# Kernel tuning notes

Hardware: AMD Instinct MI355X
Metric: run time of the kernel (lower is better)

## Reference

```python
import math
import jax, jax.numpy as jnp
import numpy as np

G, PQ, PV = 12, 4, 8

def setup_inputs() -> dict:
    key = jax.random.key(0)
    ks = jax.random.split(key, 14)
    N, L, Cn, Ce, Ch = 1, 512, 384, 128, 192
    Node = jax.random.normal(ks[0], (N, L, Cn), jnp.float32)
    Edge = jax.random.normal(ks[1], (N, L, L, Ce), jnp.float32)
    # proper rotation matrices via QR of random gaussians
    raw = jax.random.normal(ks[2], (N, L, 3, 3), jnp.float32)
    rots, _ = jnp.linalg.qr(raw)
    trans = jax.random.normal(ks[3], (N, L, 3), jnp.float32) * 10.0
    def lin(k, fan_in, fan_out):
        return jax.random.normal(k, (fan_in, fan_out), jnp.float32) / np.sqrt(fan_in)
    return {
        'Node': Node, 'Edge': Edge, 'rots': rots, 'trans': trans,
        'Wq': lin(ks[4], Cn, Ch), 'Wk': lin(ks[5], Cn, Ch), 'Wv': lin(ks[6], Cn, Ch),
        'Wqv': lin(ks[7], Cn, 3 * G * PQ), 'Wkv': lin(ks[8], Cn, 3 * G * PQ),
        'Wvv': lin(ks[9], Cn, 3 * G * PV), 'Wbias': lin(ks[10], Ce, G),
        'gamma': jnp.zeros((G,), jnp.float32),
        'Wout': lin(ks[11], Ce * G + Ch + G * PV * 4, Cn),
        'bout': jnp.zeros((Cn,), jnp.float32),
    }

def reference(Node, Edge, rots, trans, Wq, Wk, Wv, Wqv, Wkv, Wvv, Wbias, gamma, Wout, bout):
    N, L, Cn = Node.shape
    Ce = Edge.shape[-1]
    Ch = Wq.shape[1]
    ppg = Ch // G
    t = trans / 10.0  # Frame(T.rots, T.trans / 10.0)
    q = (Node @ Wq).reshape(N, L, G, ppg)
    k = (Node @ Wk).reshape(N, L, G, ppg)
    v = (Node @ Wv).reshape(N, L, G, ppg)
    qv = (Node @ Wqv).reshape(N, L, G, PQ, 3)
    kv = (Node @ Wkv).reshape(N, L, G, PQ, 3)
    vv = (Node @ Wvv).reshape(N, L, G, PV, 3)
    apply_frame = lambda p: jnp.einsum('nlij,nlgpj->nlgpi', rots, p) + t[:, :, None, None]
    qv = apply_frame(qv)
    kv = apply_frame(kv)
    vv = apply_frame(vv)
    # pairwise squared point distances, summed over xyz and query points -> [N,L,L,G]
    d = qv[:, :, None] - kv[:, None]
    sq = jnp.sum(d * d, axis=(-1, -2))
    bias = jnp.einsum('nijc,cg->nijg', Edge, Wbias)
    WC = math.sqrt(2.0 / 9.0 / PQ)
    WL = math.sqrt(1.0 / 3.0)
    attn = jnp.einsum('nlgc,nmgc->nlmg', q, k) / math.sqrt(ppg) + bias
    attn = attn - jax.nn.softplus(gamma) * (WC / 2.0) * sq
    attn = jax.nn.softmax(WL * attn, axis=2)  # softmax over key index m
    O_Edge = jnp.einsum('nijg,nijc->nigc', attn, Edge).reshape(N, L, G * Ce)
    O_Node = jnp.einsum('nijg,njgc->nigc', attn, v).reshape(N, L, Ch)
    O_vec = jnp.einsum('nijg,njgpc->nigpc', attn, vv)
    # invert_apply: R^T (x - t)
    O_vec = jnp.einsum('nlji,nlgpj->nlgpi', rots, O_vec - t[:, :, None, None])
    O_norm = jnp.sqrt(jnp.sum(O_vec * O_vec, axis=-1) + 1e-8).reshape(N, L, -1)
    O_vec = O_vec.reshape(N, L, -1)
    feat = jnp.concatenate([O_Edge, O_Node, O_vec, O_norm], axis=-1)
    return feat @ Wout + bout
```

## Files before the change

### kernel.cpp

```cpp
#include <hip/hip_runtime.h>
#include <math.h>

#define LQ 512
#define CN 384
#define CE 128
#define CH 192
#define NG 12
#define PPG 16
#define FEAT 2112
#define NPROJ 1152
#define WLs 0.5773502691896258f

#define WS_RAW  0u
#define WS_QVG  589824u
#define WS_KVT  663552u
#define WS_VVG  737280u
#define WS_QN   884736u
#define WS_KNT  890880u
#define WS_KT   897024u
#define WS_ATT  995328u
#define WS_FEAT 4141056u
#define WS_PART 5222400u
#define WS_PM   5812224u
#define WS_PS   5824512u

__global__ __launch_bounds__(256) void k1a_gemm(
    const float* __restrict__ Node,
    const float* __restrict__ Wq, const float* __restrict__ Wk,
    const float* __restrict__ Wv, const float* __restrict__ Wqv,
    const float* __restrict__ Wkv, const float* __restrict__ Wvv,
    float* __restrict__ ws)
{
    __shared__ float As[64][68];
    __shared__ float Bs[64][48];
    const int tid = threadIdx.x;
    const int cb = blockIdx.x % 24;
    const int l0 = (blockIdx.x / 24) * 64;
    const int col0 = cb * 48;

    const float* W; int nc, lc0;
    if (col0 < 192)      { W = Wq;  nc = 192; lc0 = col0; }
    else if (col0 < 384) { W = Wk;  nc = 192; lc0 = col0 - 192; }
    else if (col0 < 576) { W = Wv;  nc = 192; lc0 = col0 - 384; }
    else if (col0 < 720) { W = Wqv; nc = 144; lc0 = col0 - 576; }
    else if (col0 < 864) { W = Wkv; nc = 144; lc0 = col0 - 720; }
    else                 { W = Wvv; nc = 288; lc0 = col0 - 864; }

    const int tx = tid & 15, ty = tid >> 4;
    float acc[4][3];
#pragma unroll
    for (int r = 0; r < 4; ++r)
#pragma unroll
        for (int c = 0; c < 3; ++c) acc[r][c] = 0.f;

    for (int kc = 0; kc < 6; ++kc) {
        __syncthreads();
#pragma unroll
        for (int pass = 0; pass < 4; ++pass) {
            int m = (tid >> 4) + pass * 16;
            int kk = (tid & 15) * 4;
            const float4 a = *(const float4*)(Node + (size_t)(l0 + m) * CN + kc * 64 + kk);
            As[kk + 0][m] = a.x; As[kk + 1][m] = a.y;
            As[kk + 2][m] = a.z; As[kk + 3][m] = a.w;
        }
#pragma unroll
        for (int p = 0; p < 12; ++p) {
            int idx = p * 256 + tid;
            int kk = idx / 48, c = idx - kk * 48;
            Bs[kk][c] = W[(size_t)(kc * 64 + kk) * nc + lc0 + c];
        }
        __syncthreads();
#pragma unroll 8
        for (int kk = 0; kk < 64; ++kk) {
            const float4 av = *(const float4*)&As[kk][tx * 4];
            const float b0 = Bs[kk][ty * 3 + 0];
            const float b1 = Bs[kk][ty * 3 + 1];
            const float b2 = Bs[kk][ty * 3 + 2];
            acc[0][0] = fmaf(av.x, b0, acc[0][0]); acc[0][1] = fmaf(av.x, b1, acc[0][1]); acc[0][2] = fmaf(av.x, b2, acc[0][2]);
            acc[1][0] = fmaf(av.y, b0, acc[1][0]); acc[1][1] = fmaf(av.y, b1, acc[1][1]); acc[1][2] = fmaf(av.y, b2, acc[1][2]);
            acc[2][0] = fmaf(av.z, b0, acc[2][0]); acc[2][1] = fmaf(av.z, b1, acc[2][1]); acc[2][2] = fmaf(av.z, b2, acc[2][2]);
            acc[3][0] = fmaf(av.w, b0, acc[3][0]); acc[3][1] = fmaf(av.w, b1, acc[3][1]); acc[3][2] = fmaf(av.w, b2, acc[3][2]);
        }
    }
    float* raw = ws + WS_RAW;
#pragma unroll
    for (int r = 0; r < 4; ++r)
#pragma unroll
        for (int c = 0; c < 3; ++c)
            raw[(size_t)(l0 + tx * 4 + r) * NPROJ + col0 + ty * 3 + c] = acc[r][c];
    if (col0 >= 192 && col0 < 384) {
#pragma unroll
        for (int r = 0; r < 4; ++r)
#pragma unroll
            for (int c = 0; c < 3; ++c)
                ws[WS_KT + (size_t)(col0 - 192 + ty * 3 + c) * LQ + l0 + tx * 4 + r] = acc[r][c];
    }
}

__global__ __launch_bounds__(256) void k1b_vec(
    const float* __restrict__ rots, const float* __restrict__ trans,
    float* __restrict__ ws)
{
    __shared__ float sqbuf[96];
    const int tid = threadIdx.x;
    const int l = blockIdx.x;
    const float* raw = ws + WS_RAW + (size_t)l * NPROJ;

    if (tid < 192) {
        int src, pt, typ;
        if (tid < 48)      { typ = 0; pt = tid;      src = 576 + pt * 3; }
        else if (tid < 96) { typ = 1; pt = tid - 48; src = 720 + pt * 3; }
        else               { typ = 2; pt = tid - 96; src = 864 + pt * 3; }
        float v0 = raw[src], v1 = raw[src + 1], v2 = raw[src + 2];
        const float* R = rots + l * 9;
        float o0 = R[0] * v0 + R[1] * v1 + R[2] * v2 + trans[l * 3 + 0] * 0.1f;
        float o1 = R[3] * v0 + R[4] * v1 + R[5] * v2 + trans[l * 3 + 1] * 0.1f;
        float o2 = R[6] * v0 + R[7] * v1 + R[8] * v2 + trans[l * 3 + 2] * 0.1f;
        if (typ == 0) {
            float* dst = ws + WS_QVG + (size_t)l * 144 + pt * 3;
            dst[0] = o0; dst[1] = o1; dst[2] = o2;
        } else if (typ == 1) {
            ws[WS_KVT + (size_t)(pt * 3 + 0) * LQ + l] = o0;
            ws[WS_KVT + (size_t)(pt * 3 + 1) * LQ + l] = o1;
            ws[WS_KVT + (size_t)(pt * 3 + 2) * LQ + l] = o2;
        } else {
            float* dst = ws + WS_VVG + (size_t)l * 288 + pt * 3;
            dst[0] = o0; dst[1] = o1; dst[2] = o2;
        }
        if (tid < 96) sqbuf[tid] = o0 * o0 + o1 * o1 + o2 * o2;
    }
    __syncthreads();
    if (tid < 24) {
        int typ = tid / 12, g = tid % 12;
        int b = typ * 48 + g * 4;
        float s = sqbuf[b] + sqbuf[b + 1] + sqbuf[b + 2] + sqbuf[b + 3];
        if (typ == 0) ws[WS_QN + (size_t)l * 12 + g] = s;
        else          ws[WS_KNT + (size_t)g * LQ + l] = s;
    }
}

__global__ __launch_bounds__(256, 4) void k2_attn(
    const float* __restrict__ Edge, const float* __restrict__ Wbias,
    const float* __restrict__ gamma, float* __restrict__ ws)
{
    __shared__ float et[256 * 33];
    __shared__ float cgls[NG];
    __shared__ float red[4][NG];
    const int tid = threadIdx.x;
    const int i = blockIdx.x >> 1;
    const int h = blockIdx.x & 1;
    const int j = h * 256 + tid;

    if (tid < NG)
        cgls[tid] = log1pf(__expf(gamma[tid])) * 0.11785113019775793f;

    const float4* e4 = (const float4*)Edge + ((size_t)i * LQ + h * 256) * 32;
    float4 buf[8];
#pragma unroll
    for (int kk = 0; kk < 8; ++kk) {
        int idx = kk * 256 + tid;
        buf[kk] = e4[(size_t)(idx >> 3) * 32 + (idx & 7)];
    }
    __syncthreads();

    float lgs[NG];
    {
        const float* qrow  = ws + WS_RAW + (size_t)i * NPROJ;
        const float* qvrow = ws + WS_QVG + (size_t)i * 144;
        const float* qnrow = ws + WS_QN  + (size_t)i * NG;
        const float* KT  = ws + WS_KT;
        const float* KVT = ws + WS_KVT;
        const float* KNT = ws + WS_KNT;
#pragma unroll
        for (int g = 0; g < NG; ++g) {
            float qk = 0.f;
#pragma unroll
            for (int u = 0; u < PPG; ++u)
                qk = fmaf(qrow[g * PPG + u], KT[(size_t)(g * PPG + u) * LQ + j], qk);
            float dt = 0.f;
#pragma unroll
            for (int u = 0; u < 12; ++u)
                dt = fmaf(qvrow[g * 12 + u], KVT[(size_t)(g * 12 + u) * LQ + j], dt);
            float sq = qnrow[g] + KNT[(size_t)g * LQ + j] - 2.f * dt;
            lgs[g] = qk * 0.25f - cgls[g] * sq;
        }
    }

#pragma unroll
    for (int kk = 0; kk < 8; ++kk) {
        int idx = kk * 256 + tid;
        float* d = et + (idx >> 3) * 33 + (idx & 7) * 4;
        d[0] = buf[kk].x; d[1] = buf[kk].y; d[2] = buf[kk].z; d[3] = buf[kk].w;
    }
    __syncthreads();

    for (int ch = 0; ch < 4; ++ch) {
        if (ch < 3) {
#pragma unroll
            for (int kk = 0; kk < 8; ++kk) {
                int idx = kk * 256 + tid;
                buf[kk] = e4[(size_t)(idx >> 3) * 32 + (ch + 1) * 8 + (idx & 7)];
            }
        }
        const float* wbch = Wbias + ch * 32 * NG;
        const float* r0 = et + tid * 33;
#pragma unroll 4
        for (int c = 0; c < 32; ++c) {
            float e0 = r0[c];
            const float* wb = wbch + c * NG;
#pragma unroll
            for (int g = 0; g < NG; ++g) lgs[g] = fmaf(e0, wb[g], lgs[g]);
        }
        __syncthreads();
        if (ch < 3) {
#pragma unroll
            for (int kk = 0; kk < 8; ++kk) {
                int idx = kk * 256 + tid;
                float* d = et + (idx >> 3) * 33 + (idx & 7) * 4;
                d[0] = buf[kk].x; d[1] = buf[kk].y; d[2] = buf[kk].z; d[3] = buf[kk].w;
            }
            __syncthreads();
        }
    }

    const int wid = tid >> 6, lane = tid & 63;
    float pm[NG];
#pragma unroll
    for (int g = 0; g < NG; ++g) pm[g] = lgs[g];
#pragma unroll
    for (int g = 0; g < NG; ++g)
        for (int off = 1; off < 64; off <<= 1)
            pm[g] = fmaxf(pm[g], __shfl_xor(pm[g], off));
    if (lane == 0) {
#pragma unroll
        for (int g = 0; g < NG; ++g) red[wid][g] = pm[g];
    }
    __syncthreads();
    float gm[NG];
#pragma unroll
    for (int g = 0; g < NG; ++g)
        gm[g] = fmaxf(fmaxf(red[0][g], red[1][g]), fmaxf(red[2][g], red[3][g]));
    if (tid < NG)
        ws[WS_PM + ((size_t)i * 2 + h) * NG + tid] =
            fmaxf(fmaxf(red[0][tid], red[1][tid]), fmaxf(red[2][tid], red[3][tid]));
    __syncthreads();

    float ps[NG];
#pragma unroll
    for (int g = 0; g < NG; ++g) {
        float e = __expf(WLs * (lgs[g] - gm[g]));
        lgs[g] = e;
        ps[g] = e;
    }
#pragma unroll
    for (int g = 0; g < NG; ++g)
        for (int off = 1; off < 64; off <<= 1)
            ps[g] += __shfl_xor(ps[g], off);
    if (lane == 0) {
#pragma unroll
        for (int g = 0; g < NG; ++g) red[wid][g] = ps[g];
    }
    __syncthreads();
    if (tid < NG)
        ws[WS_PS + ((size_t)i * 2 + h) * NG + tid] =
            red[0][tid] + red[1][tid] + red[2][tid] + red[3][tid];

    float* attT = ws + WS_ATT + (size_t)i * (NG * LQ);
#pragma unroll
    for (int g = 0; g < NG; ++g) attT[g * LQ + j] = lgs[g];
}

__global__ __launch_bounds__(256) void k3a_oedge(
    const float* __restrict__ Edge, float* __restrict__ ws)
{
    __shared__ float atls[NG * 516];
    __shared__ float bufA[4][32][NG][4];
    __shared__ float sc[2][NG];
    const int tid = threadIdx.x;
    const int qi = blockIdx.x;

    if (tid < 24) {
        int hh = tid / NG, g = tid % NG;
        float m0 = ws[WS_PM + ((size_t)qi * 2 + 0) * NG + g];
        float m1 = ws[WS_PM + ((size_t)qi * 2 + 1) * NG + g];
        float ss0 = ws[WS_PS + ((size_t)qi * 2 + 0) * NG + g];
        float ss1 = ws[WS_PS + ((size_t)qi * 2 + 1) * NG + g];
        float m = fmaxf(m0, m1);
        float e0 = __expf(WLs * (m0 - m));
        float e1 = __expf(WLs * (m1 - m));
        float denom = ss0 * e0 + ss1 * e1;
        sc[hh][g] = (hh ? e1 : e0) / denom;
    }
    __syncthreads();

    const float4* attT4 = (const float4*)(ws + WS_ATT + (size_t)qi * (NG * LQ));
#pragma unroll
    for (int m = 0; m < 6; ++m) {
        int idx = m * 256 + tid;
        int g = idx >> 7, j4 = idx & 127;
        float s = sc[j4 >> 6][g];
        float4 v = attT4[g * 128 + j4];
        v.x *= s; v.y *= s; v.z *= s; v.w *= s;
        *(float4*)&atls[g * 516 + j4 * 4] = v;
    }
    __syncthreads();

    const int w = tid >> 6, lane = tid & 63, jh = lane >> 5, c4 = lane & 31;
    float acc[NG][4];
#pragma unroll
    for (int g = 0; g < NG; ++g)
#pragma unroll
        for (int r = 0; r < 4; ++r) acc[g][r] = 0.f;
    const float4* e4 = (const float4*)(Edge + (size_t)qi * LQ * CE);
    for (int s = 0; s < 16; ++s) {
        int j0 = w * 128 + jh * 64 + s * 4;
        float4 e0 = e4[(size_t)(j0 + 0) * 32 + c4];
        float4 e1 = e4[(size_t)(j0 + 1) * 32 + c4];
        float4 e2 = e4[(size_t)(j0 + 2) * 32 + c4];
        float4 e3 = e4[(size_t)(j0 + 3) * 32 + c4];
#pragma unroll
        for (int g = 0; g < NG; ++g) {
            float4 a = *(const float4*)&atls[g * 516 + j0];
            acc[g][0] = fmaf(a.x, e0.x, fmaf(a.y, e1.x, fmaf(a.z, e2.x, fmaf(a.w, e3.x, acc[g][0]))));
            acc[g][1] = fmaf(a.x, e0.y, fmaf(a.y, e1.y, fmaf(a.z, e2.y, fmaf(a.w, e3.y, acc[g][1]))));
            acc[g][2] = fmaf(a.x, e0.z, fmaf(a.y, e1.z, fmaf(a.z, e2.z, fmaf(a.w, e3.z, acc[g][2]))));
            acc[g][3] = fmaf(a.x, e0.w, fmaf(a.y, e1.w, fmaf(a.z, e2.w, fmaf(a.w, e3.w, acc[g][3]))));
        }
    }
#pragma unroll
    for (int g = 0; g < NG; ++g)
#pragma unroll
        for (int r = 0; r < 4; ++r) acc[g][r] += __shfl_xor(acc[g][r], 32);
    if (jh == 0) {
#pragma unroll
        for (int g = 0; g < NG; ++g)
#pragma unroll
            for (int r = 0; r < 4; ++r) bufA[w][c4][g][r] = acc[g][r];
    }
    __syncthreads();
    float* feat = ws + WS_FEAT + (size_t)qi * FEAT;
    for (int m = 0; m < 6; ++m) {
        int o = tid + m * 256;
        int g = o >> 7, c = o & 127;
        int cc4 = c >> 2, r = c & 3;
        feat[o] = bufA[0][cc4][g][r] + bufA[1][cc4][g][r] +
                  bufA[2][cc4][g][r] + bufA[3][cc4][g][r];
    }
}

__global__ __launch_bounds__(256) void k3b_rest(
    const float* __restrict__ rots, const float* __restrict__ trans,
    float* __restrict__ ws)
{
    __shared__ float atls[NG * 516];
    __shared__ float sc[2][NG];
    __shared__ float ovecl[240];
    const int tid = threadIdx.x;
    const int qi = blockIdx.x >> 1;
    const int s  = blockIdx.x & 1;

    if (tid < 24) {
        int hh = tid / NG, g = tid % NG;
        float m0 = ws[WS_PM + ((size_t)qi * 2 + 0) * NG + g];
        float m1 = ws[WS_PM + ((size_t)qi * 2 + 1) * NG + g];
        float ss0 = ws[WS_PS + ((size_t)qi * 2 + 0) * NG + g];
        float ss1 = ws[WS_PS + ((size_t)qi * 2 + 1) * NG + g];
        float m = fmaxf(m0, m1);
        float e0 = __expf(WLs * (m0 - m));
        float e1 = __expf(WLs * (m1 - m));
        float denom = ss0 * e0 + ss1 * e1;
        sc[hh][g] = (hh ? e1 : e0) / denom;
    }
    __syncthreads();

    const float4* attT4 = (const float4*)(ws + WS_ATT + (size_t)qi * (NG * LQ));
#pragma unroll
    for (int m = 0; m < 6; ++m) {
        int idx = m * 256 + tid;
        int g = idx >> 7, j4 = idx & 127;
        float f = sc[j4 >> 6][g];
        float4 v = attT4[g * 128 + j4];
        v.x *= f; v.y *= f; v.z *= f; v.w *= f;
        *(float4*)&atls[g * 516 + j4 * 4] = v;
    }
    __syncthreads();

    float* feat = ws + WS_FEAT + (size_t)qi * FEAT;
    const float* raw = ws + WS_RAW;
    const float* vvg = ws + WS_VVG;
    if (tid < 240) {
        if (s == 0 && tid < 192) {
            int g = tid >> 4;
            const float* arow = atls + g * 516;
            float sum = 0.f;
            for (int j4 = 0; j4 < 128; ++j4) {
                float4 a = *(const float4*)&arow[j4 * 4];
                int j = j4 * 4;
                sum = fmaf(a.x, raw[(size_t)(j + 0) * NPROJ + 384 + tid], sum);
                sum = fmaf(a.y, raw[(size_t)(j + 1) * NPROJ + 384 + tid], sum);
                sum = fmaf(a.z, raw[(size_t)(j + 2) * NPROJ + 384 + tid], sum);
                sum = fmaf(a.w, raw[(size_t)(j + 3) * NPROJ + 384 + tid], sum);
            }
            feat[1536 + tid] = sum;
        } else {
            int u = (s == 0) ? (tid - 192) : (48 + tid);
            int lidx = (s == 0) ? (tid - 192) : tid;
            int g = u / 24;
            const float* arow = atls + g * 516;
            float sum = 0.f;
            for (int j4 = 0; j4 < 128; ++j4) {
                float4 a = *(const float4*)&arow[j4 * 4];
                int j = j4 * 4;
                sum = fmaf(a.x, vvg[(size_t)(j + 0) * 288 + u], sum);
                sum = fmaf(a.y, vvg[(size_t)(j + 1) * 288 + u], sum);
                sum = fmaf(a.z, vvg[(size_t)(j + 2) * 288 + u], sum);
                sum = fmaf(a.w, vvg[(size_t)(j + 3) * 288 + u], sum);
            }
            ovecl[lidx] = sum;
        }
    }
    __syncthreads();

    int npts = (s == 0) ? 16 : 80;
    if (tid < npts) {
        int P = (s == 0) ? tid : (16 + tid);
        int u0l = (s == 0) ? (P * 3) : (P * 3 - 48);
        const float* R = rots + qi * 9;
        float t0 = trans[qi * 3 + 0] * 0.1f;
        float t1 = trans[qi * 3 + 1] * 0.1f;
        float t2 = trans[qi * 3 + 2] * 0.1f;
        float d0 = ovecl[u0l + 0] - t0;
        float d1 = ovecl[u0l + 1] - t1;
        float d2 = ovecl[u0l + 2] - t2;
        float o0 = R[0] * d0 + R[3] * d1 + R[6] * d2;
        float o1 = R[1] * d0 + R[4] * d1 + R[7] * d2;
        float o2 = R[2] * d0 + R[5] * d1 + R[8] * d2;
        feat[1728 + P * 3 + 0] = o0;
        feat[1728 + P * 3 + 1] = o1;
        feat[1728 + P * 3 + 2] = o2;
        feat[2016 + P] = sqrtf(o0 * o0 + o1 * o1 + o2 * o2 + 1e-8f);
    }
}

__global__ __launch_bounds__(256) void k4_gemm(const float* __restrict__ Wout,
                                               float* __restrict__ ws)
{
    __shared__ float As[64][68];
    __shared__ float Bs[64][48];
    const int tid = threadIdx.x;
    const int cc = blockIdx.x >> 6;
    const int t  = blockIdx.x & 63;
    const int l0 = (t >> 3) * 64;
    const int col0 = (t & 7) * 48;
    const float* feat = ws + WS_FEAT;

    const int tx = tid & 15, ty = tid >> 4;
    float acc[4][3];
#pragma unroll
    for (int r = 0; r < 4; ++r)
#pragma unroll
        for (int c = 0; c < 3; ++c) acc[r][c] = 0.f;

    for (int kc = cc * 11; kc < cc * 11 + 11; ++kc) {
        __syncthreads();
#pragma unroll
        for (int pass = 0; pass < 4; ++pass) {
            int m = (tid >> 4) + pass * 16;
            int kk = (tid & 15) * 4;
            const float4 a = *(const float4*)(feat + (size_t)(l0 + m) * FEAT + kc * 64 + kk);
            As[kk + 0][m] = a.x; As[kk + 1][m] = a.y;
            As[kk + 2][m] = a.z; As[kk + 3][m] = a.w;
        }
#pragma unroll
        for (int p = 0; p < 12; ++p) {
            int idx = p * 256 + tid;
            int kk = idx / 48, c = idx - kk * 48;
            Bs[kk][c] = Wout[(size_t)(kc * 64 + kk) * CN + col0 + c];
        }
        __syncthreads();
#pragma unroll 8
        for (int kk = 0; kk < 64; ++kk) {
            const float4 av = *(const float4*)&As[kk][tx * 4];
            const float b0 = Bs[kk][ty * 3 + 0];
            const float b1 = Bs[kk][ty * 3 + 1];
            const float b2 = Bs[kk][ty * 3 + 2];
            acc[0][0] = fmaf(av.x, b0, acc[0][0]); acc[0][1] = fmaf(av.x, b1, acc[0][1]); acc[0][2] = fmaf(av.x, b2, acc[0][2]);
            acc[1][0] = fmaf(av.y, b0, acc[1][0]); acc[1][1] = fmaf(av.y, b1, acc[1][1]); acc[1][2] = fmaf(av.y, b2, acc[1][2]);
            acc[2][0] = fmaf(av.z, b0, acc[2][0]); acc[2][1] = fmaf(av.z, b1, acc[2][1]); acc[2][2] = fmaf(av.z, b2, acc[2][2]);
            acc[3][0] = fmaf(av.w, b0, acc[3][0]); acc[3][1] = fmaf(av.w, b1, acc[3][1]); acc[3][2] = fmaf(av.w, b2, acc[3][2]);
        }
    }
    float* part = ws + WS_PART + (size_t)cc * LQ * CN;
#pragma unroll
    for (int r = 0; r < 4; ++r)
#pragma unroll
        for (int c = 0; c < 3; ++c)
            part[(size_t)(l0 + tx * 4 + r) * CN + col0 + ty * 3 + c] = acc[r][c];
}

__global__ __launch_bounds__(384) void k5_red(const float* __restrict__ bout,
                                              const float* __restrict__ wsc,
                                              float* __restrict__ out)
{
    const int i = blockIdx.x, n = threadIdx.x;
    const float* part = wsc + WS_PART;
    size_t idx = (size_t)i * CN + n;
    size_t st = (size_t)LQ * CN;
    out[idx] = part[idx] + part[st + idx] + part[2 * st + idx] + bout[n];
}

extern "C" void kernel_launch(void* const* d_in, const int* in_sizes, int n_in,
                              void* d_out, int out_size, void* d_ws, size_t ws_size,
                              hipStream_t stream) {
    const float* Node  = (const float*)d_in[0];
    const float* Edge  = (const float*)d_in[1];
    const float* rots  = (const float*)d_in[2];
    const float* trans = (const float*)d_in[3];
    const float* Wq    = (const float*)d_in[4];
    const float* Wk    = (const float*)d_in[5];
    const float* Wv    = (const float*)d_in[6];
    const float* Wqv   = (const float*)d_in[7];
    const float* Wkv   = (const float*)d_in[8];
    const float* Wvv   = (const float*)d_in[9];
    const float* Wbias = (const float*)d_in[10];
    const float* gamma = (const float*)d_in[11];
    const float* Wout  = (const float*)d_in[12];
    const float* bout  = (const float*)d_in[13];
    float* ws = (float*)d_ws;

    k1a_gemm<<<192, 256, 0, stream>>>(Node, Wq, Wk, Wv, Wqv, Wkv, Wvv, ws);
    k1b_vec<<<512, 256, 0, stream>>>(rots, trans, ws);
    k2_attn<<<1024, 256, 0, stream>>>(Edge, Wbias, gamma, ws);
    k3a_oedge<<<512, 256, 0, stream>>>(Edge, ws);
    k3b_rest<<<1024, 256, 0, stream>>>(rots, trans, ws);
    k4_gemm<<<192, 256, 0, stream>>>(Wout, ws);
    k5_red<<<512, 384, 0, stream>>>(bout, ws, (float*)d_out);
}
```

Measured before the change: 189.6 us.

## Split O_Edge kernel over key halves and stage Wbias in shared memory

```diff
diff --git a/kernel.cpp b/kernel.cpp
--- a/kernel.cpp
+++ b/kernel.cpp
@@ -23,6 +23,7 @@
 #define WS_PART 5222400u
 #define WS_PM   5812224u
 #define WS_PS   5824512u
+#define WS_OE2  5836800u
 
 __global__ __launch_bounds__(256) void k1a_gemm(
     const float* __restrict__ Node,
@@ -144,6 +145,7 @@
     const float* __restrict__ gamma, float* __restrict__ ws)
 {
     __shared__ float et[256 * 33];
+    __shared__ float wbs[NG * CE];
     __shared__ float cgls[NG];
     __shared__ float red[4][NG];
     const int tid = threadIdx.x;
@@ -153,6 +155,10 @@
 
     if (tid < NG)
         cgls[tid] = log1pf(__expf(gamma[tid])) * 0.11785113019775793f;
+    for (int u = tid; u < NG * CE; u += 256) {
+        int c = u / NG, g = u - c * NG;
+        wbs[g * CE + c] = Wbias[u];
+    }
 
     const float4* e4 = (const float4*)Edge + ((size_t)i * LQ + h * 256) * 32;
     float4 buf[8];
@@ -202,14 +208,17 @@
                 buf[kk] = e4[(size_t)(idx >> 3) * 32 + (ch + 1) * 8 + (idx & 7)];
             }
         }
-        const float* wbch = Wbias + ch * 32 * NG;
         const float* r0 = et + tid * 33;
-#pragma unroll 4
-        for (int c = 0; c < 32; ++c) {
-            float e0 = r0[c];
-            const float* wb = wbch + c * NG;
-#pragma unroll
-            for (int g = 0; g < NG; ++g) lgs[g] = fmaf(e0, wb[g], lgs[g]);
+#pragma unroll
+        for (int c4 = 0; c4 < 8; ++c4) {
+            float e0 = r0[c4 * 4 + 0], e1 = r0[c4 * 4 + 1];
+            float e2 = r0[c4 * 4 + 2], e3 = r0[c4 * 4 + 3];
+#pragma unroll
+            for (int g = 0; g < NG; ++g) {
+                const float4 wv = *(const float4*)&wbs[g * CE + ch * 32 + c4 * 4];
+                lgs[g] = fmaf(e0, wv.x, fmaf(e1, wv.y,
+                         fmaf(e2, wv.z, fmaf(e3, wv.w, lgs[g]))));
+            }
         }
         __syncthreads();
         if (ch < 3) {
@@ -273,14 +282,15 @@
 __global__ __launch_bounds__(256) void k3a_oedge(
     const float* __restrict__ Edge, float* __restrict__ ws)
 {
-    __shared__ float atls[NG * 516];
+    __shared__ float atls[NG * 260];
     __shared__ float bufA[4][32][NG][4];
-    __shared__ float sc[2][NG];
-    const int tid = threadIdx.x;
-    const int qi = blockIdx.x;
-
-    if (tid < 24) {
-        int hh = tid / NG, g = tid % NG;
+    __shared__ float scl[NG];
+    const int tid = threadIdx.x;
+    const int qi = blockIdx.x >> 1;
+    const int half = blockIdx.x & 1;
+
+    if (tid < NG) {
+        int g = tid;
         float m0 = ws[WS_PM + ((size_t)qi * 2 + 0) * NG + g];
         float m1 = ws[WS_PM + ((size_t)qi * 2 + 1) * NG + g];
         float ss0 = ws[WS_PS + ((size_t)qi * 2 + 0) * NG + g];
@@ -289,19 +299,19 @@
         float e0 = __expf(WLs * (m0 - m));
         float e1 = __expf(WLs * (m1 - m));
         float denom = ss0 * e0 + ss1 * e1;
-        sc[hh][g] = (hh ? e1 : e0) / denom;
+        scl[g] = (half ? e1 : e0) / denom;
     }
     __syncthreads();
 
     const float4* attT4 = (const float4*)(ws + WS_ATT + (size_t)qi * (NG * LQ));
 #pragma unroll
-    for (int m = 0; m < 6; ++m) {
+    for (int m = 0; m < 3; ++m) {
         int idx = m * 256 + tid;
-        int g = idx >> 7, j4 = idx & 127;
-        float s = sc[j4 >> 6][g];
-        float4 v = attT4[g * 128 + j4];
+        int g = idx >> 6, j4l = idx & 63;
+        float s = scl[g];
+        float4 v = attT4[g * 128 + half * 64 + j4l];
         v.x *= s; v.y *= s; v.z *= s; v.w *= s;
-        *(float4*)&atls[g * 516 + j4 * 4] = v;
+        *(float4*)&atls[g * 260 + j4l * 4] = v;
     }
     __syncthreads();
 
@@ -311,16 +321,16 @@
     for (int g = 0; g < NG; ++g)
 #pragma unroll
         for (int r = 0; r < 4; ++r) acc[g][r] = 0.f;
-    const float4* e4 = (const float4*)(Edge + (size_t)qi * LQ * CE);
-    for (int s = 0; s < 16; ++s) {
-        int j0 = w * 128 + jh * 64 + s * 4;
+    const float4* e4 = (const float4*)(Edge + ((size_t)qi * LQ + half * 256) * CE);
+    for (int s = 0; s < 8; ++s) {
+        int j0 = w * 64 + jh * 32 + s * 4;
         float4 e0 = e4[(size_t)(j0 + 0) * 32 + c4];
         float4 e1 = e4[(size_t)(j0 + 1) * 32 + c4];
         float4 e2 = e4[(size_t)(j0 + 2) * 32 + c4];
         float4 e3 = e4[(size_t)(j0 + 3) * 32 + c4];
 #pragma unroll
         for (int g = 0; g < NG; ++g) {
-            float4 a = *(const float4*)&atls[g * 516 + j0];
+            float4 a = *(const float4*)&atls[g * 260 + j0];
             acc[g][0] = fmaf(a.x, e0.x, fmaf(a.y, e1.x, fmaf(a.z, e2.x, fmaf(a.w, e3.x, acc[g][0]))));
             acc[g][1] = fmaf(a.x, e0.y, fmaf(a.y, e1.y, fmaf(a.z, e2.y, fmaf(a.w, e3.y, acc[g][1]))));
             acc[g][2] = fmaf(a.x, e0.z, fmaf(a.y, e1.z, fmaf(a.z, e2.z, fmaf(a.w, e3.z, acc[g][2]))));
@@ -338,13 +348,27 @@
             for (int r = 0; r < 4; ++r) bufA[w][c4][g][r] = acc[g][r];
     }
     __syncthreads();
-    float* feat = ws + WS_FEAT + (size_t)qi * FEAT;
+    float* oe2 = ws + WS_OE2 + ((size_t)qi * 2 + half) * 1536;
     for (int m = 0; m < 6; ++m) {
         int o = tid + m * 256;
         int g = o >> 7, c = o & 127;
         int cc4 = c >> 2, r = c & 3;
-        feat[o] = bufA[0][cc4][g][r] + bufA[1][cc4][g][r] +
-                  bufA[2][cc4][g][r] + bufA[3][cc4][g][r];
+        oe2[o] = bufA[0][cc4][g][r] + bufA[1][cc4][g][r] +
+                 bufA[2][cc4][g][r] + bufA[3][cc4][g][r];
+    }
+}
+
+__global__ __launch_bounds__(256) void k3c_merge(float* __restrict__ ws)
+{
+    const int tid = threadIdx.x;
+    const int qi = blockIdx.x;
+    const float* p0 = ws + WS_OE2 + (size_t)qi * 2 * 1536;
+    const float* p1 = p0 + 1536;
+    float* feat = ws + WS_FEAT + (size_t)qi * FEAT;
+#pragma unroll
+    for (int m = 0; m < 6; ++m) {
+        int o = m * 256 + tid;
+        feat[o] = p0[o] + p1[o];
     }
 }
 
@@ -531,8 +555,9 @@
     k1a_gemm<<<192, 256, 0, stream>>>(Node, Wq, Wk, Wv, Wqv, Wkv, Wvv, ws);
     k1b_vec<<<512, 256, 0, stream>>>(rots, trans, ws);
     k2_attn<<<1024, 256, 0, stream>>>(Edge, Wbias, gamma, ws);
-    k3a_oedge<<<512, 256, 0, stream>>>(Edge, ws);
+    k3a_oedge<<<1024, 256, 0, stream>>>(Edge, ws);
     k3b_rest<<<1024, 256, 0, stream>>>(rots, trans, ws);
+    k3c_merge<<<512, 256, 0, stream>>>(ws);
     k4_gemm<<<192, 256, 0, stream>>>(Wout, ws);
     k5_red<<<512, 384, 0, stream>>>(bout, ws, (float*)d_out);
 }
```

After: 198.1 us. 4.5% more time.
